# Kernel tuning notes

Hardware: AMD Instinct MI355X
Metric: run time of the kernel (lower is better)

Reference implementation:

```python
import jax, jax.numpy as jnp
import numpy as np
from jax import lax

EPS = 1e-5
H = 4      # num_heads
D = 64     # qkv_dim (== in_channels)


def _bn(x, gamma, beta, mean, var):
    # eval-mode BatchNorm2d over NCHW, channel axis 1
    inv = gamma / jnp.sqrt(var + EPS)
    return x * inv[:, None, None] + (beta - mean * inv)[:, None, None]


def _conv(x, w, b, pad_w):
    y = lax.conv_general_dilated(x, w, window_strides=(1, 1),
                                 padding=[(0, 0), (pad_w, pad_w)],
                                 dimension_numbers=("NCHW", "OIHW", "NCHW"))
    return y + b[None, :, None, None]


def setup_inputs() -> dict:
    key = jax.random.key(0)
    ks = jax.random.split(key, 16)
    N, C, T, V = 16, 64, 64, 25
    s = 0.05
    return {
        "x": jax.random.normal(ks[0], (N, C, T, V), jnp.float32),
        "W_qkv": jax.random.normal(ks[1], (C, 3 * H * D), jnp.float32) * s,
        "b_qkv": jax.random.normal(ks[2], (3 * H * D,), jnp.float32) * s,
        "W_out": jax.random.normal(ks[3], (C, C * H, 1, 9), jnp.float32) * s,
        "b_out": jax.random.normal(ks[4], (C,), jnp.float32) * s,
        "bn1_gamma": jax.random.uniform(ks[5], (C,), jnp.float32) + 0.5,
        "bn1_beta": jax.random.normal(ks[6], (C,), jnp.float32) * s,
        "bn1_mean": jax.random.normal(ks[7], (C,), jnp.float32) * s,
        "bn1_var": jax.random.uniform(ks[8], (C,), jnp.float32) + 0.5,
        "W_ff": jax.random.normal(ks[9], (C, C, 1, 1), jnp.float32) * s,
        "b_ff": jax.random.normal(ks[10], (C,), jnp.float32) * s,
        "bn2_gamma": jax.random.uniform(ks[11], (C,), jnp.float32) + 0.5,
        "bn2_beta": jax.random.normal(ks[12], (C,), jnp.float32) * s,
        "bn2_mean": jax.random.normal(ks[13], (C,), jnp.float32) * s,
        "bn2_var": jax.random.uniform(ks[14], (C,), jnp.float32) + 0.5,
    }


def reference(x, W_qkv, b_qkv, W_out, b_out, bn1_gamma, bn1_beta, bn1_mean,
              bn1_var, W_ff, b_ff, bn2_gamma, bn2_beta, bn2_mean, bn2_var):
    N, C, T, V = x.shape
    L = T * V
    # qkv projection on [N,T,V,C]
    xt = jnp.transpose(x, (0, 2, 3, 1))                        # [N,T,V,C]
    qkv = xt.reshape(N, L, C) @ W_qkv + b_qkv                  # [N,L,3*H*D]
    qkv = qkv.reshape(N, L, 3, H, D)
    q = jnp.transpose(qkv[:, :, 0], (0, 2, 1, 3))              # [N,H,L,D]
    k = jnp.transpose(qkv[:, :, 1], (0, 2, 1, 3))              # [N,H,L,D]
    v = jnp.transpose(qkv[:, :, 2], (0, 2, 1, 3))              # [N,H,L,D]
    attn = jnp.einsum("nhld,nhmd->nhlm", q, k) / jnp.sqrt(jnp.float32(D))
    attn = jax.nn.softmax(attn, axis=-1)
    o = jnp.einsum("nhlm,nhmd->nhld", attn, v)                 # [N,H,L,D]
    # view(N,H,T,V,D).permute(0,1,4,2,3).view(N,H*D,T,V)
    o = o.reshape(N, H, T, V, D)
    o = jnp.transpose(o, (0, 1, 4, 2, 3)).reshape(N, H * D, T, V)
    # out_nets: Conv2d (1,9) pad (0,4) + BN, residual (identity), relu
    y = _bn(_conv(o, W_out, b_out, 4), bn1_gamma, bn1_beta, bn1_mean, bn1_var)
    y = jax.nn.relu(y + x)
    # ff_net: 1x1 conv + BN, residual, relu
    z = _bn(_conv(y, W_ff, b_ff, 0), bn2_gamma, bn2_beta, bn2_mean, bn2_var)
    return jax.nn.relu(z + y)
```

## Files before the change

### kernel.cpp

```cpp
#include <hip/hip_runtime.h>
#include <hip/hip_bf16.h>

#define NB 16
#define CC 64
#define TT 64
#define VV 25
#define LL 1600
#define HH 4
#define DD 64
#define NH 64


typedef __hip_bfloat16 bf16;
typedef __attribute__((ext_vector_type(8))) short short8;
typedef __attribute__((ext_vector_type(4))) float f32x4;
typedef __attribute__((ext_vector_type(4))) int int4v;
typedef __attribute__((ext_vector_type(4))) unsigned short us4;

__device__ __forceinline__ float b2f(bf16 v) { return __bfloat162float(v); }
__device__ __forceinline__ unsigned short f2bf_bits(float f) {
  bf16 h = __float2bfloat16(f);
  return *(unsigned short*)&h;
}
__device__ __forceinline__ unsigned pkbf_trunc(float lo, float hi) {
  return __builtin_amdgcn_perm(__float_as_uint(hi), __float_as_uint(lo), 0x07060302u);
}
__device__ __forceinline__ float dppx1(float x) {
  return __int_as_float(
      __builtin_amdgcn_mov_dpp(__float_as_int(x), 0xB1, 0xF, 0xF, true));
}
__device__ __forceinline__ int dppx1i(int x) {
  return __builtin_amdgcn_mov_dpp(x, 0xB1, 0xF, 0xF, true);
}
__device__ __forceinline__ void pl32swap(int &a, int &b) {
  asm("v_permlane32_swap_b32 %0, %1" : "+v"(a), "+v"(b));
}
__device__ __forceinline__ void pl16swap(int &a, int &b) {
  asm("v_permlane16_swap_b32 %0, %1" : "+v"(a), "+v"(b));
}

__global__ void k_prep(const float* __restrict__ Wo, const float* __restrict__ Wf,
                       const float* __restrict__ Wq,
                       bf16* __restrict__ Wt, bf16* __restrict__ WfT,
                       bf16* __restrict__ WqT) {
  int i = blockIdx.x * 256 + threadIdx.x;
  if (i < 147456) {
    int j = i & 7, lane = (i >> 3) & 63, cot = (i >> 9) & 3;
    int kc = (i >> 11) & 7, r = i >> 14;
    int co = cot * 16 + (lane & 15);
    int ci = kc * 32 + (lane >> 4) * 8 + j;
    Wt[i] = __float2bfloat16(Wo[(co * 256 + ci) * 9 + r]);
  }
  if (i < 4096) {
    int j = i & 7, lane = (i >> 3) & 63, cot = (i >> 9) & 3, kc = (i >> 11) & 1;
    int co = cot * 16 + (lane & 15);
    int ci = kc * 32 + (lane >> 4) * 8 + j;
    WfT[i] = __float2bfloat16(Wf[co * 64 + ci]);
  }
  if (i < 49152) {
    int jj = i & 7, lane = (i >> 3) & 63, g = i >> 9;
    int nt = g % 48, half = g / 48;
    int ch = half * 32 + (lane >> 4) * 8 + jj;
    int j = nt * 16 + (lane & 15);
    WqT[i] = __float2bfloat16(Wq[ch * 768 + j]);
  }
}

__global__ __launch_bounds__(256)
void k_qkv(const float* __restrict__ x, const bf16* __restrict__ WqT,
           const float* __restrict__ bq,
           bf16* __restrict__ q, bf16* __restrict__ k, bf16* __restrict__ vt) {
  __shared__ short xa_all[4][16 * 72];
  __shared__ short tr_all[4][16 * 66];
  int tid = threadIdx.x;
  int wv = tid >> 6, lane = tid & 63;
  int quad = lane >> 4, c = lane & 15;
  int g4 = blockIdx.x * 4 + wv;
  int n = g4 / 100;
  int l0 = (g4 % 100) * 16;
  short* xa = xa_all[wv];
  short* tr = tr_all[wv];
  bool ev = (c & 1) == 0;

  {
    int l = c;
    const float* xb = x + (size_t)n * 102400 + (size_t)(quad * 16) * 1600 + l0 + l;
    unsigned short vb[16];
#pragma unroll
    for (int i = 0; i < 16; i++) vb[i] = f2bf_bits(xb[(size_t)i * 1600]);
    unsigned wrds[8];
#pragma unroll
    for (int i = 0; i < 8; i++)
      wrds[i] = ((unsigned)vb[2 * i + 1] << 16) | vb[2 * i];
    *(short8*)(xa + l * 72 + quad * 16) = *(short8*)&wrds[0];
    *(short8*)(xa + l * 72 + quad * 16 + 8) = *(short8*)&wrds[4];
  }
  asm volatile("" ::: "memory");
  short8 af0 = *(const short8*)(xa + c * 72 + quad * 8);
  short8 af1 = *(const short8*)(xa + c * 72 + 32 + quad * 8);

  const short* wq0 = (const short*)WqT;
  const float QSCALE = 0.125f * 1.44269504f;

  short8 bc[8], bn[8];
#pragma unroll
  for (int t = 0; t < 4; t++) {
    bc[2 * t]     = *(const short8*)(wq0 + ((size_t)t * 64 + lane) * 8);
    bc[2 * t + 1] = *(const short8*)(wq0 + ((size_t)(48 + t) * 64 + lane) * 8);
  }

#pragma unroll
  for (int g = 0; g < 12; g++) {
    int s = g >> 2, h = g & 3;
    f32x4 z[4];
#pragma unroll
    for (int t = 0; t < 4; t++) {
      int nt = g * 4 + t;
      float bv = bq[nt * 16 + c];
      f32x4 zz = {bv, bv, bv, bv};
      zz = __builtin_amdgcn_mfma_f32_16x16x32_bf16(af0, bc[2 * t], zz, 0, 0, 0);
      zz = __builtin_amdgcn_mfma_f32_16x16x32_bf16(af1, bc[2 * t + 1], zz, 0, 0, 0);
      z[t] = zz;
    }
    if (g < 11) {
#pragma unroll
      for (int t = 0; t < 4; t++) {
        int nt = (g + 1) * 4 + t;
        bn[2 * t]     = *(const short8*)(wq0 + ((size_t)nt * 64 + lane) * 8);
        bn[2 * t + 1] = *(const short8*)(wq0 + ((size_t)(48 + nt) * 64 + lane) * 8);
      }
    }
    if (s < 2) {
      asm volatile("" ::: "memory");
#pragma unroll
      for (int t = 0; t < 4; t++) {
        if (s == 0) {
#pragma unroll
          for (int r = 0; r < 4; r++) z[t][r] *= QSCALE;
        }
        int us_[4];
#pragma unroll
        for (int r = 0; r < 4; r++) us_[r] = f2bf_bits(z[t][r]);
        int xv0 = dppx1i(us_[0]);
        int xv1 = dppx1i(us_[1]);
        int xv2 = dppx1i(us_[2]);
        int xv3 = dppx1i(us_[3]);
        if (ev) {
          *(int*)(tr + (quad * 4 + 0) * 66 + t * 16 + c) = (xv0 << 16) | us_[0];
          *(int*)(tr + (quad * 4 + 1) * 66 + t * 16 + c) = (xv1 << 16) | us_[1];
        } else {
          *(int*)(tr + (quad * 4 + 2) * 66 + t * 16 + (c - 1)) = (us_[2] << 16) | xv2;
          *(int*)(tr + (quad * 4 + 3) * 66 + t * 16 + (c - 1)) = (us_[3] << 16) | xv3;
        }
      }
      asm volatile("" ::: "memory");
      int row = lane >> 2, seg = lane & 3;
      short8 o0 = *(const short8*)(tr + row * 66 + seg * 16);
      short8 o1 = *(const short8*)(tr + row * 66 + seg * 16 + 8);
      short* dstp = (short*)(s == 0 ? q : k);
      short* dst = dstp + ((size_t)(n * 4 + h) * 1600 + l0 + row) * 64 + seg * 16;
      *(short8*)(dst) = o0;
      *(short8*)(dst + 8) = o1;
      asm volatile("" ::: "memory");
    } else {
#pragma unroll
      for (int t = 0; t < 4; t++) {
        us4 pk;
#pragma unroll
        for (int r = 0; r < 4; r++) pk[r] = f2bf_bits(z[t][r]);
        *(us4*)((short*)vt + ((size_t)((n * 4 + h) * 64 + t * 16 + c)) * 1600 +
                l0 + quad * 4) = pk;
      }
    }
#pragma unroll
    for (int i = 0; i < 8; i++) bc[i] = bn[i];
  }
}

__global__ __launch_bounds__(256, 2)
void k_attn(const bf16* __restrict__ q, const bf16* __restrict__ k,
            const bf16* __restrict__ vt, bf16* __restrict__ po,
            float* __restrict__ ls, int split) {
  __shared__ short kbuf[64 * 72];
  __shared__ short vbuf[64 * 72];
  __shared__ short pl_all[4][16 * 66];
  int tid = threadIdx.x;
  int wv = tid >> 6, lane = tid & 63;
  int quad = lane >> 4, c = lane & 15;
  int bid = blockIdx.x;
  int xcd = bid & 7;
  int slot = bid >> 3;
  int half, qt, grp;
  if (split == 2) { half = slot & 1; qt = (slot >> 1) % 25; grp = slot / 50; }
  else            { half = 0;        qt = slot % 25;        grp = slot / 25; }
  int nh = grp * 8 + xcd;
  int kt0 = half ? 13 : 0;
  int kt1 = (split == 2 && half == 0) ? 13 : 25;
  int l0 = qt * 64 + wv * 16;
  short* pl = pl_all[wv];

  const short* qbase = (const short*)q + ((size_t)nh * 1600 + l0 + c) * 64 + quad * 8;
  short8 qf0 = *(const short8*)(qbase);
  short8 qf1 = *(const short8*)(qbase + 32);

  short ob = (c == 0) ? (short)0x3F80 : (short)0;
  short8 onesf = {ob, ob, ob, ob, ob, ob, ob, ob};

  f32x4 acc[5] = {};

  const short* kg = (const short*)k + (size_t)nh * 102400;
  const short* vg = (const short*)vt + (size_t)nh * 102400;
  bool ev = (c & 1) == 0;

  short8 sk[2], sv[2];
  {
    const short8* gk = (const short8*)(kg + kt0 * 4096);
#pragma unroll
    for (int i = 0; i < 2; i++) sk[i] = gk[tid + i * 256];
#pragma unroll
    for (int i = 0; i < 2; i++) {
      int ch = tid + i * 256;
      sv[i] = *(const short8*)(vg + (size_t)(ch >> 3) * 1600 + kt0 * 64 + (ch & 7) * 8);
    }
  }

  for (int kt = kt0; kt < kt1; kt++) {
    __syncthreads();
#pragma unroll
    for (int i = 0; i < 2; i++) {
      int ch = tid + i * 256;
      *(short8*)(kbuf + (ch >> 3) * 72 + (ch & 7) * 8) = sk[i];
      *(short8*)(vbuf + (ch >> 3) * 72 + (ch & 7) * 8) = sv[i];
    }
    __syncthreads();
    if (kt + 1 < kt1) {
      const short8* gk = (const short8*)(kg + (kt + 1) * 4096);
#pragma unroll
      for (int i = 0; i < 2; i++) sk[i] = gk[tid + i * 256];
#pragma unroll
      for (int i = 0; i < 2; i++) {
        int ch = tid + i * 256;
        sv[i] = *(const short8*)(vg + (size_t)(ch >> 3) * 1600 + (kt + 1) * 64 + (ch & 7) * 8);
      }
    }
    f32x4 s[4];
#pragma unroll
    for (int ct = 0; ct < 4; ct++) {
      short8 kf0 = *(const short8*)(kbuf + (ct * 16 + c) * 72 + quad * 8);
      short8 kf1 = *(const short8*)(kbuf + (ct * 16 + c) * 72 + 32 + quad * 8);
      f32x4 z0 = {-8.f, -8.f, -8.f, -8.f};
      z0 = __builtin_amdgcn_mfma_f32_16x16x32_bf16(kf0, qf0, z0, 0, 0, 0);
      z0 = __builtin_amdgcn_mfma_f32_16x16x32_bf16(kf1, qf1, z0, 0, 0, 0);
      s[ct] = z0;
    }
#pragma unroll
    for (int ct = 0; ct < 4; ct++)
#pragma unroll
      for (int r = 0; r < 4; r++) s[ct][r] = exp2f(s[ct][r]);
    short8 vf[4][2];
#pragma unroll
    for (int ct = 0; ct < 4; ct++) {
      vf[ct][0] = *(const short8*)(vbuf + (ct * 16 + c) * 72 + quad * 8);
      vf[ct][1] = *(const short8*)(vbuf + (ct * 16 + c) * 72 + 32 + quad * 8);
    }
    {
      int wA[4], wB[4];
#pragma unroll
      for (int ct = 0; ct < 4; ct++) {
        wA[ct] = (int)pkbf_trunc(s[ct][0], s[ct][1]);
        wB[ct] = (int)pkbf_trunc(s[ct][2], s[ct][3]);
      }
      pl32swap(wA[0], wA[1]); pl16swap(wA[0], wA[1]);
      pl32swap(wB[0], wB[1]); pl16swap(wB[0], wB[1]);
      int4v f0 = {wA[0], wB[0], wA[1], wB[1]};
      pl32swap(wA[2], wA[3]); pl16swap(wA[2], wA[3]);
      pl32swap(wB[2], wB[3]); pl16swap(wB[2], wB[3]);
      int4v f1 = {wA[2], wB[2], wA[3], wB[3]};
      short8 pf0 = *(short8*)&f0;
      short8 pf1 = *(short8*)&f1;
#pragma unroll
      for (int ct = 0; ct < 4; ct++) {
        acc[ct] = __builtin_amdgcn_mfma_f32_16x16x32_bf16(pf0, vf[ct][0], acc[ct], 0, 0, 0);
        acc[ct] = __builtin_amdgcn_mfma_f32_16x16x32_bf16(pf1, vf[ct][1], acc[ct], 0, 0, 0);
      }
      acc[4] = __builtin_amdgcn_mfma_f32_16x16x32_bf16(pf0, onesf, acc[4], 0, 0, 0);
      acc[4] = __builtin_amdgcn_mfma_f32_16x16x32_bf16(pf1, onesf, acc[4], 0, 0, 0);
    }
  }
  int n = nh >> 2, h = nh & 3;
  {
    float linv[4] = {1.f, 1.f, 1.f, 1.f};
    if (split == 1) {
#pragma unroll
      for (int r = 0; r < 4; r++)
        linv[r] = 1.0f / __shfl(acc[4][r], lane & 48);
    }
    asm volatile("" ::: "memory");
#pragma unroll
    for (int t = 0; t < 4; t++) {
      int us_[4];
#pragma unroll
      for (int r = 0; r < 4; r++) us_[r] = f2bf_bits(acc[t][r] * linv[r]);
      int xv0 = dppx1i(us_[0]);
      int xv1 = dppx1i(us_[1]);
      int xv2 = dppx1i(us_[2]);
      int xv3 = dppx1i(us_[3]);
      if (ev) {
        *(int*)(pl + (quad * 4 + 0) * 66 + t * 16 + c) = (xv0 << 16) | us_[0];
        *(int*)(pl + (quad * 4 + 1) * 66 + t * 16 + c) = (xv1 << 16) | us_[1];
      } else {
        *(int*)(pl + (quad * 4 + 2) * 66 + t * 16 + (c - 1)) = (us_[2] << 16) | xv2;
        *(int*)(pl + (quad * 4 + 3) * 66 + t * 16 + (c - 1)) = (us_[3] << 16) | xv3;
      }
    }
    asm volatile("" ::: "memory");
    int row = lane >> 2, seg = lane & 3;
    short8 o0 = *(const short8*)(pl + row * 66 + seg * 16);
    short8 o1 = *(const short8*)(pl + row * 66 + seg * 16 + 8);
    short* dst = (short*)po + (size_t)half * 6553600 +
                 ((size_t)n * 1600 + l0 + row) * 256 + h * 64 + seg * 16;
    *(short8*)(dst) = o0;
    *(short8*)(dst + 8) = o1;
    if (split == 2 && c == 0) {
#pragma unroll
      for (int r = 0; r < 4; r++)
        ls[half * 102400 + nh * 1600 + l0 + quad * 4 + r] = acc[4][r];
    }
    asm volatile("" ::: "memory");
  }
}

__global__ void k_comb(const bf16* po_in, const float* __restrict__ ls, bf16* ot) {
  int i = blockIdx.x * 256 + threadIdx.x;
  int ch8 = i & 31;
  int rest = i >> 5;
  int l = rest % 1600;
  int n = rest / 1600;
  int nh = n * 4 + (ch8 >> 3);
  float inv = 1.0f / (ls[nh * 1600 + l] + ls[102400 + nh * 1600 + l]);
  const short* a = (const short*)po_in + (size_t)rest * 256 + ch8 * 8;
  short8 av = *(const short8*)a;
  short8 bv = *(const short8*)(a + 6553600);
  unsigned short o8[8];
#pragma unroll
  for (int j = 0; j < 8; j++) {
    float fa = __uint_as_float(((unsigned)(unsigned short)av[j]) << 16);
    float fb = __uint_as_float(((unsigned)(unsigned short)bv[j]) << 16);
    o8[j] = f2bf_bits((fa + fb) * inv);
  }
  *(short8*)((short*)ot + (size_t)rest * 256 + ch8 * 8) = *(short8*)o8;
}

__global__ __launch_bounds__(256)
void k_conv9(const bf16* __restrict__ ot, const bf16* __restrict__ Wt,
             const float* __restrict__ bo, const float* __restrict__ g1,
             const float* __restrict__ be1, const float* __restrict__ mu1,
             const float* __restrict__ va1, const float* __restrict__ x,
             const bf16* __restrict__ WfT, const float* __restrict__ bff,
             const float* __restrict__ g2, const float* __restrict__ be2,
             const float* __restrict__ mu2, const float* __restrict__ va2,
             float* __restrict__ out) {
  __shared__ short tl[4][16 * 66];
  int tid = threadIdx.x;
  int wv = tid >> 6;
  int lane = tid & 63;
  int quad = lane >> 4, c = lane & 15;
  int n = blockIdx.y;
  int l0 = blockIdx.x * 64 + wv * 16;
  int la = l0 + c;
  int va = la % 25;
  const short* obase = (const short*)ot + (size_t)n * 409600;
  const short* wbase = (const short*)Wt;
  f32x4 acc[4] = {};
  for (int r = 0; r < 9; r++) {
    int sh = r - 4;
    bool valid = (unsigned)(va + sh) < 25u;
    int lp = la + sh;
    lp = max(0, min(1599, lp));
    const short* arow = obase + (size_t)lp * 256 + quad * 8;
    const short* wrow = wbase + (size_t)r * 8 * 4 * 64 * 8 + lane * 8;
    short8 z8 = {0, 0, 0, 0, 0, 0, 0, 0};
#pragma unroll 4
    for (int kc = 0; kc < 8; kc++) {
      short8 af = *(const short8*)(arow + kc * 32);
      af = valid ? af : z8;
      const short* wk = wrow + kc * 4 * 64 * 8;
      short8 b0 = *(const short8*)(wk);
      short8 b1 = *(const short8*)(wk + 512);
      short8 b2 = *(const short8*)(wk + 1024);
      short8 b3 = *(const short8*)(wk + 1536);
      acc[0] = __builtin_amdgcn_mfma_f32_16x16x32_bf16(af, b0, acc[0], 0, 0, 0);
      acc[1] = __builtin_amdgcn_mfma_f32_16x16x32_bf16(af, b1, acc[1], 0, 0, 0);
      acc[2] = __builtin_amdgcn_mfma_f32_16x16x32_bf16(af, b2, acc[2], 0, 0, 0);
      acc[3] = __builtin_amdgcn_mfma_f32_16x16x32_bf16(af, b3, acc[3], 0, 0, 0);
    }
  }
  short* tlw = &tl[wv][0];
  float outv[4][4];
#pragma unroll
  for (int cot = 0; cot < 4; cot++) {
    int co = cot * 16 + c;
    float inv = g1[co] * rsqrtf(va1[co] + 1e-5f);
    float add = be1[co] - mu1[co] * inv + bo[co] * inv;
    f32x4 xr = *(const f32x4*)(x + (size_t)(n * 64 + co) * 1600 + l0 + quad * 4);
#pragma unroll
    for (int rr = 0; rr < 4; rr++)
      outv[cot][rr] = fmaxf(acc[cot][rr] * inv + add + xr[rr], 0.f);
  }
  asm volatile("" ::: "memory");
  bool ev = (c & 1) == 0;
#pragma unroll
  for (int cot = 0; cot < 4; cot++) {
    int us_[4];
#pragma unroll
    for (int rr = 0; rr < 4; rr++) us_[rr] = f2bf_bits(outv[cot][rr]);
    int xv0 = dppx1i(us_[0]);
    int xv1 = dppx1i(us_[1]);
    int xv2 = dppx1i(us_[2]);
    int xv3 = dppx1i(us_[3]);
    if (ev) {
      *(int*)(tlw + (quad * 4 + 0) * 66 + cot * 16 + c) = (xv0 << 16) | us_[0];
      *(int*)(tlw + (quad * 4 + 1) * 66 + cot * 16 + c) = (xv1 << 16) | us_[1];
    } else {
      *(int*)(tlw + (quad * 4 + 2) * 66 + cot * 16 + (c - 1)) = (us_[2] << 16) | xv2;
      *(int*)(tlw + (quad * 4 + 3) * 66 + cot * 16 + (c - 1)) = (us_[3] << 16) | xv3;
    }
  }
  asm volatile("" ::: "memory");
  short8 afY0 = *(const short8*)(tlw + c * 66 + quad * 8);
  short8 afY1 = *(const short8*)(tlw + c * 66 + 32 + quad * 8);
  const short* wfb = (const short*)WfT + lane * 8;
  f32x4 acc2[4] = {};
#pragma unroll
  for (int kc = 0; kc < 2; kc++) {
    short8 afk = kc ? afY1 : afY0;
    const short* wk = wfb + kc * 2048;
    short8 b0 = *(const short8*)(wk);
    short8 b1 = *(const short8*)(wk + 512);
    short8 b2 = *(const short8*)(wk + 1024);
    short8 b3 = *(const short8*)(wk + 1536);
    acc2[0] = __builtin_amdgcn_mfma_f32_16x16x32_bf16(afk, b0, acc2[0], 0, 0, 0);
    acc2[1] = __builtin_amdgcn_mfma_f32_16x16x32_bf16(afk, b1, acc2[1], 0, 0, 0);
    acc2[2] = __builtin_amdgcn_mfma_f32_16x16x32_bf16(afk, b2, acc2[2], 0, 0, 0);
    acc2[3] = __builtin_amdgcn_mfma_f32_16x16x32_bf16(afk, b3, acc2[3], 0, 0, 0);
  }
#pragma unroll
  for (int cot = 0; cot < 4; cot++) {
    int co = cot * 16 + c;
    float inv = g2[co] * rsqrtf(va2[co] + 1e-5f);
    float add = be2[co] - mu2[co] * inv + bff[co] * inv;
    f32x4 ov;
#pragma unroll
    for (int rr = 0; rr < 4; rr++)
      ov[rr] = fmaxf(acc2[cot][rr] * inv + add + outv[cot][rr], 0.f);
    *(f32x4*)(out + (size_t)(n * 64 + co) * 1600 + l0 + quad * 4) = ov;
  }
}

extern "C" void kernel_launch(void* const* d_in, const int* in_sizes, int n_in,
                              void* d_out, int out_size, void* d_ws, size_t ws_size,
                              hipStream_t stream) {
  const float* x   = (const float*)d_in[0];
  const float* Wq  = (const float*)d_in[1];
  const float* bq  = (const float*)d_in[2];
  const float* Wo  = (const float*)d_in[3];
  const float* bo  = (const float*)d_in[4];
  const float* g1  = (const float*)d_in[5];
  const float* be1 = (const float*)d_in[6];
  const float* mu1 = (const float*)d_in[7];
  const float* va1 = (const float*)d_in[8];
  const float* Wf  = (const float*)d_in[9];
  const float* bff = (const float*)d_in[10];
  const float* g2  = (const float*)d_in[11];
  const float* be2 = (const float*)d_in[12];
  const float* mu2 = (const float*)d_in[13];
  const float* va2 = (const float*)d_in[14];

  const size_t QKV = (size_t)64 * 1600 * 64;
  size_t elems2 = 5 * QKV + 147456 + 4096 + 49152;
  size_t need2 = elems2 * 2 + 2 * 102400 * 4 + 256;
  int split = (ws_size >= need2) ? 2 : 1;

  bf16* qw  = (bf16*)d_ws;
  bf16* kw  = qw + QKV;
  bf16* vtw = kw + QKV;
  bf16* pow_ = vtw + QKV;
  bf16* Wt  = pow_ + (size_t)split * QKV;
  bf16* WfT = Wt + 147456;
  bf16* WqT = WfT + 4096;
  float* ls = (float*)(WqT + 49152);

  k_prep<<<576, 256, 0, stream>>>(Wo, Wf, Wq, Wt, WfT, WqT);
  k_qkv<<<400, 256, 0, stream>>>(x, WqT, bq, qw, kw, vtw);
  k_attn<<<split * 1600, 256, 0, stream>>>(qw, kw, vtw, pow_, ls, split);
  if (split == 2) k_comb<<<3200, 256, 0, stream>>>(pow_, ls, pow_);
  dim3 gc(25, 16);
  k_conv9<<<gc, 256, 0, stream>>>(pow_, Wt, bo, g1, be1, mu1, va1, x,
                                  WfT, bff, g2, be2, mu2, va2, (float*)d_out);
}
```

Measured before the change: 220.7 us.

## Merge two attention heads per 512-thread block with shared LDS region

The attention kernel now runs 512-thread blocks, each processing two (batch, head) pairs: the two halves of the block use separate K/V tiles in one shared LDS array. The per-wave P scratch aliases that same LDS array, so a barrier is added before the epilogue. Half as many blocks are launched. The aim is to cut LDS footprint per head and improve occupancy and scheduling. The risks are larger barrier scopes across 8 waves and the dropped min-blocks launch bound, which may change register allocation.

Result: slower. 235.5 us (+6.7%).

```diff
diff --git a/kernel.cpp b/kernel.cpp
--- a/kernel.cpp
+++ b/kernel.cpp
@@ -177,27 +177,28 @@
   }
 }
 
-__global__ __launch_bounds__(256, 2)
+__global__ __launch_bounds__(512)
 void k_attn(const bf16* __restrict__ q, const bf16* __restrict__ k,
             const bf16* __restrict__ vt, bf16* __restrict__ po,
             float* __restrict__ ls, int split) {
-  __shared__ short kbuf[64 * 72];
-  __shared__ short vbuf[64 * 72];
-  __shared__ short pl_all[4][16 * 66];
+  __shared__ short smem[2][2][64 * 72];
   int tid = threadIdx.x;
   int wv = tid >> 6, lane = tid & 63;
   int quad = lane >> 4, c = lane & 15;
+  int hi = wv >> 2, wq = wv & 3;
   int bid = blockIdx.x;
   int xcd = bid & 7;
   int slot = bid >> 3;
-  int half, qt, grp;
-  if (split == 2) { half = slot & 1; qt = (slot >> 1) % 25; grp = slot / 50; }
-  else            { half = 0;        qt = slot % 25;        grp = slot / 25; }
-  int nh = grp * 8 + xcd;
+  int half, qt, jp;
+  if (split == 2) { half = slot & 1; qt = (slot >> 1) % 25; jp = slot / 50; }
+  else            { half = 0;        qt = slot % 25;        jp = slot / 25; }
+  int nh = xcd + 8 * (jp + 4 * hi);
   int kt0 = half ? 13 : 0;
   int kt1 = (split == 2 && half == 0) ? 13 : 25;
-  int l0 = qt * 64 + wv * 16;
-  short* pl = pl_all[wv];
+  int l0 = qt * 64 + wq * 16;
+  short* kbuf = &smem[hi][0][0];
+  short* vbuf = &smem[hi][1][0];
+  short* pl = ((short*)smem) + wv * 2112;
 
   const short* qbase = (const short*)q + ((size_t)nh * 1600 + l0 + c) * 64 + quad * 8;
   short8 qf0 = *(const short8*)(qbase);
@@ -212,14 +213,15 @@
   const short* vg = (const short*)vt + (size_t)nh * 102400;
   bool ev = (c & 1) == 0;
 
+  int t256 = tid & 255;
   short8 sk[2], sv[2];
   {
     const short8* gk = (const short8*)(kg + kt0 * 4096);
 #pragma unroll
-    for (int i = 0; i < 2; i++) sk[i] = gk[tid + i * 256];
+    for (int i = 0; i < 2; i++) sk[i] = gk[t256 + i * 256];
 #pragma unroll
     for (int i = 0; i < 2; i++) {
-      int ch = tid + i * 256;
+      int ch = t256 + i * 256;
       sv[i] = *(const short8*)(vg + (size_t)(ch >> 3) * 1600 + kt0 * 64 + (ch & 7) * 8);
     }
   }
@@ -228,7 +230,7 @@
     __syncthreads();
 #pragma unroll
     for (int i = 0; i < 2; i++) {
-      int ch = tid + i * 256;
+      int ch = t256 + i * 256;
       *(short8*)(kbuf + (ch >> 3) * 72 + (ch & 7) * 8) = sk[i];
       *(short8*)(vbuf + (ch >> 3) * 72 + (ch & 7) * 8) = sv[i];
     }
@@ -236,10 +238,10 @@
     if (kt + 1 < kt1) {
       const short8* gk = (const short8*)(kg + (kt + 1) * 4096);
 #pragma unroll
-      for (int i = 0; i < 2; i++) sk[i] = gk[tid + i * 256];
+      for (int i = 0; i < 2; i++) sk[i] = gk[t256 + i * 256];
 #pragma unroll
       for (int i = 0; i < 2; i++) {
-        int ch = tid + i * 256;
+        int ch = t256 + i * 256;
         sv[i] = *(const short8*)(vg + (size_t)(ch >> 3) * 1600 + (kt + 1) * 64 + (ch & 7) * 8);
       }
     }
@@ -287,6 +289,7 @@
       acc[4] = __builtin_amdgcn_mfma_f32_16x16x32_bf16(pf1, onesf, acc[4], 0, 0, 0);
     }
   }
+  __syncthreads();
   int n = nh >> 2, h = nh & 3;
   {
     float linv[4] = {1.f, 1.f, 1.f, 1.f};
@@ -492,7 +495,7 @@
 
   k_prep<<<576, 256, 0, stream>>>(Wo, Wf, Wq, Wt, WfT, WqT);
   k_qkv<<<400, 256, 0, stream>>>(x, WqT, bq, qw, kw, vtw);
-  k_attn<<<split * 1600, 256, 0, stream>>>(qw, kw, vtw, pow_, ls, split);
+  k_attn<<<split * 800, 512, 0, stream>>>(qw, kw, vtw, pow_, ls, split);
   if (split == 2) k_comb<<<3200, 256, 0, stream>>>(pow_, ls, pow_);
   dim3 gc(25, 16);
   k_conv9<<<gc, 256, 0, stream>>>(pow_, Wt, bo, g1, be1, mu1, va1, x,
```
